# Kernel tuning notes

Measured on AMD Instinct MI355X. Metric: run time of the kernel, lower is better.

The kernel has to match this reference:

```python
import jax, jax.numpy as jnp
import numpy as np

BLOCK = 32  # block_h == block_w (triton blocksparse requires square blocks)


def setup_inputs() -> dict:
    key = jax.random.key(0)
    kq, kk, kv, kb, km = jax.random.split(key, 5)
    B, H, S, D = 2, 16, 2048, 64
    query = jax.random.normal(kq, (B, H, S, D), dtype=jnp.float32)
    key_t = jax.random.normal(kk, (B, H, S, D), dtype=jnp.float32)
    value = jax.random.normal(kv, (B, H, S, D), dtype=jnp.float32)
    # grouped Conv2d bias (default bias=True, left at random init in the module)
    conv_bias = jax.random.normal(kb, (H,), dtype=jnp.float32)
    mask = jax.random.randint(km, (H, S, S), 0, 2, dtype=jnp.int32)
    return {"query": query, "key": key_t, "value": value,
            "conv_bias": conv_bias, "mask": mask}


def reference(query, key, value, conv_bias, mask):
    # --- build data-dependent block mask (grouped conv, weight==1, stride==kernel==BLOCK) ---
    H, S, _ = mask.shape
    nb = S // BLOCK
    block_sum = mask.reshape(H, nb, BLOCK, nb, BLOCK).sum(axis=(2, 4)).astype(jnp.float32)
    block_mask = (block_sum + conv_bias[:, None, None]) > 0  # [H, nb, nb]

    # element-level allowed pattern: block active AND causal (triton sparse_softmax is_causal=True)
    elem = jnp.repeat(jnp.repeat(block_mask, BLOCK, axis=1), BLOCK, axis=2)  # [H, S, S]
    causal = jnp.tril(jnp.ones((S, S), dtype=bool))
    allow = elem & causal  # [H, S, S]

    # --- sparse SDD: QK^T restricted to active blocks (scale = 1.0) ---
    scores = jnp.einsum('bhsd,bhtd->bhst', query, key)  # [B, H, S, S]

    # --- sparse causal softmax: disallowed positions are -inf; fully-masked rows -> 0 ---
    NEG = jnp.float32(-1e30)
    s = jnp.where(allow[None], scores, NEG)
    m = jnp.max(s, axis=-1, keepdims=True)
    p = jnp.where(allow[None], jnp.exp(s - m), 0.0)
    denom = jnp.sum(p, axis=-1, keepdims=True)
    w = jnp.where(denom > 0, p / denom, 0.0)

    # --- sparse DSD: attention @ V (absent blocks contribute zero) ---
    return jnp.einsum('bhst,bhtd->bhsd', w, value)
```

## Files before the change

### kernel.cpp

```cpp
#include <hip/hip_runtime.h>
#include <hip/hip_bf16.h>


typedef _Float16 f16_t;
typedef f16_t  f16x8  __attribute__((ext_vector_type(8)));
typedef __fp16 fp16x2 __attribute__((ext_vector_type(2)));
typedef float  f32x4  __attribute__((ext_vector_type(4)));
typedef float  f32x16 __attribute__((ext_vector_type(16)));
typedef int    i32x4  __attribute__((ext_vector_type(4)));
typedef int    i32x2  __attribute__((ext_vector_type(2)));
typedef unsigned int u32x4 __attribute__((ext_vector_type(4)));

constexpr int Bc = 2, Hc = 16, Sc = 2048, Dc = 64;
constexpr int NB = Sc / 32;
constexpr float LOG2E = 1.4426950408889634f;
constexpr size_t FRAG_BH = (size_t)NB * 4 * 64 * 8;

__device__ inline f32x16 mfma32(f16x8 a, f16x8 b, f32x16 c) {
    return __builtin_amdgcn_mfma_f32_32x32x16_f16(a, b, c, 0, 0, 0);
}
__device__ inline float fexp2(float x) { return __builtin_amdgcn_exp2f(x); }

union UB { u32x4 u; f16x8 v; };
union PK { fp16x2 h; unsigned int u; };

#if __has_builtin(__builtin_amdgcn_permlane32_swap)
#define HAVE_PLSWAP 1
__device__ inline i32x2 plswap(unsigned int a, unsigned int b) {
    return __builtin_amdgcn_permlane32_swap((int)a, (int)b, false, false);
}
__device__ inline float xhalf_max(float x) {
    i32x2 s = plswap((unsigned int)__float_as_int(x), (unsigned int)__float_as_int(x));
    return fmaxf(__int_as_float(s[0]), __int_as_float(s[1]));
}
__device__ inline float xhalf_sum(float x) {
    i32x2 s = plswap((unsigned int)__float_as_int(x), (unsigned int)__float_as_int(x));
    return __int_as_float(s[0]) + __int_as_float(s[1]);
}
#else
#define HAVE_PLSWAP 0
__device__ inline float xhalf_max(float x) { return fmaxf(x, __shfl_xor(x, 32)); }
__device__ inline float xhalf_sum(float x) { return x + __shfl_xor(x, 32); }
#endif

__global__ __launch_bounds__(256) void k_prep(const float* __restrict__ K,
                                              const float* __restrict__ V,
                                              const int* __restrict__ mask,
                                              const float* __restrict__ bias,
                                              f16_t* __restrict__ khf,
                                              f16_t* __restrict__ vaf,
                                              unsigned char* __restrict__ bm) {
    __shared__ f16_t tile[32 * 66];
    const int bid = blockIdx.x;
    const int t   = threadIdx.x;
    if (bid < 2048) {
        const int bh = bid >> 6, kb = bid & 63;
        const float* src = K + ((size_t)bh * Sc + (size_t)kb * 32) * Dc;
        {
            int r = t >> 3, c8 = (t & 7) * 8;
            f32x4 a = *(const f32x4*)(src + r * Dc + c8);
            f32x4 b = *(const f32x4*)(src + r * Dc + c8 + 4);
            float xs[8] = {a[0], a[1], a[2], a[3], b[0], b[1], b[2], b[3]};
#pragma unroll
            for (int j = 0; j < 8; j++) tile[r * 66 + c8 + j] = (f16_t)xs[j];
        }
        __syncthreads();
        {
            int kc = t >> 6, lane = t & 63, l31 = lane & 31, hi2 = (lane >> 5) & 1;
            f16x8 frag;
#pragma unroll
            for (int j = 0; j < 8; j++)
                frag[j] = tile[l31 * 66 + kc * 16 + hi2 * 8 + j];
            *(f16x8*)(khf + (((size_t)(bh * NB + kb) * 4 + kc) * 64 + lane) * 8) = frag;
        }
    } else if (bid < 4096) {
        const int b2 = bid - 2048;
        const int bh = b2 >> 6, kb = b2 & 63;
        const float* src = V + ((size_t)bh * Sc + (size_t)kb * 32) * Dc;
        {
            int r = t >> 3, c8 = (t & 7) * 8;
            f32x4 a = *(const f32x4*)(src + r * Dc + c8);
            f32x4 b = *(const f32x4*)(src + r * Dc + c8 + 4);
            float xs[8] = {a[0], a[1], a[2], a[3], b[0], b[1], b[2], b[3]};
#pragma unroll
            for (int j = 0; j < 8; j++) tile[r * 66 + c8 + j] = (f16_t)xs[j];
        }
        __syncthreads();
        {
            int f = t >> 6, lane = t & 63, l31 = lane & 31, hi2 = (lane >> 5) & 1;
            int tt = f >> 1, c = f & 1;
            f16x8 frag;
#pragma unroll
            for (int j = 0; j < 8; j++)
                frag[j] = tile[(c * 16 + hi2 * 8 + j) * 66 + tt * 32 + l31];
            *(f16x8*)(vaf + (((size_t)(bh * NB + kb) * 4 + f) * 64 + lane) * 8) = frag;
        }
    } else {
        const int b3 = bid - 4096;
        const int h  = b3 >> 6;
        const int br = b3 & 63;
        float bv = bias[h];
        unsigned char* outp = bm + ((size_t)h * NB + br) * NB;
        if (bv > 0.f) {
            if (t < NB) outp[t] = 1;
            return;
        }
        int bc0 = t >> 3;
        int bc1 = 32 + bc0;
        const int* base = mask + ((size_t)h * Sc + (size_t)br * 32) * (size_t)Sc;
        const int* p0 = base + 4 * t;
        const int* p1 = base + 1024 + 4 * t;
        bool d0 = (bc0 <= br), d1 = (bc1 <= br);
        int acc0 = 0, acc1 = 0;
        if (d0) {
#pragma unroll
            for (int r = 0; r < 4; r++) {
                i32x4 vv = *(const i32x4*)(p0 + (size_t)r * Sc);
                acc0 += vv[0] + vv[1] + vv[2] + vv[3];
            }
        }
        if (d1) {
#pragma unroll
            for (int r = 0; r < 4; r++) {
                i32x4 vv = *(const i32x4*)(p1 + (size_t)r * Sc);
                acc1 += vv[0] + vv[1] + vv[2] + vv[3];
            }
        }
        int g0 = acc0, g1 = acc1;
#pragma unroll
        for (int off = 1; off < 8; off <<= 1) {
            g0 += __shfl_xor(g0, off);
            g1 += __shfl_xor(g1, off);
        }
        bool act0 = (float)g0 + bv > 0.f;
        bool act1 = (float)g1 + bv > 0.f;
        if (d0 && !act0) {
            for (int r = 4; r < 32; r++) {
                i32x4 vv = *(const i32x4*)(p0 + (size_t)r * Sc);
                acc0 += vv[0] + vv[1] + vv[2] + vv[3];
            }
            int s = acc0;
#pragma unroll
            for (int off = 1; off < 8; off <<= 1) s += __shfl_xor(s, off);
            act0 = (float)s + bv > 0.f;
        }
        if (d1 && !act1) {
            for (int r = 4; r < 32; r++) {
                i32x4 vv = *(const i32x4*)(p1 + (size_t)r * Sc);
                acc1 += vv[0] + vv[1] + vv[2] + vv[3];
            }
            int s = acc1;
#pragma unroll
            for (int off = 1; off < 8; off <<= 1) s += __shfl_xor(s, off);
            act1 = (float)s + bv > 0.f;
        }
        if ((t & 7) == 0) {
            if (d0) outp[bc0] = act0 ? 1 : 0;
            if (d1) outp[bc1] = act1 ? 1 : 0;
        }
    }
}

#if HAVE_PLSWAP
#define EXCHANGE_P(PB, B0, B1) do {                                            \
        i32x2 e0_ = plswap(PB[0], PB[2]);                                      \
        i32x2 e1_ = plswap(PB[1], PB[3]);                                      \
        i32x2 e2_ = plswap(PB[4], PB[6]);                                      \
        i32x2 e3_ = plswap(PB[5], PB[7]);                                      \
        B0.u[0] = (unsigned int)e0_[0]; B0.u[1] = (unsigned int)e1_[0];        \
        B0.u[2] = (unsigned int)e0_[1]; B0.u[3] = (unsigned int)e1_[1];        \
        B1.u[0] = (unsigned int)e2_[0]; B1.u[1] = (unsigned int)e3_[0];        \
        B1.u[2] = (unsigned int)e2_[1]; B1.u[3] = (unsigned int)e3_[1];        \
} while (0)
#else
#define EXCHANGE_P(PB, B0, B1) do {                                            \
        unsigned int qb_[8];                                                   \
        _Pragma("unroll")                                                      \
        for (int i_ = 0; i_ < 8; i_++)                                         \
            qb_[i_] = (unsigned int)__shfl_xor((int)PB[i_], 32);               \
        B0.u[0] = hi ? qb_[2] : PB[0]; B0.u[1] = hi ? qb_[3] : PB[1];          \
        B0.u[2] = hi ? PB[2] : qb_[0]; B0.u[3] = hi ? PB[3] : qb_[1];          \
        B1.u[0] = hi ? qb_[6] : PB[4]; B1.u[1] = hi ? qb_[7] : PB[5];          \
        B1.u[2] = hi ? PB[6] : qb_[4]; B1.u[3] = hi ? PB[7] : qb_[5];          \
} while (0)
#endif

#define CORE(OT0, OT1, MR, LR, QH, BROW, kb_) do {                             \
        f32x16 st;                                                             \
        _Pragma("unroll")                                                      \
        for (int r_ = 0; r_ < 16; r_++) st[r_] = 0.f;                          \
        _Pragma("unroll")                                                      \
        for (int kc_ = 0; kc_ < 4; kc_++)                                      \
            st = mfma32(kbuf_[kc_], QH[kc_], st);                              \
        if ((kb_) == (BROW)) {                                                 \
            _Pragma("unroll")                                                  \
            for (int r_ = 0; r_ < 16; r_++) {                                  \
                int kvl_ = (r_ & 3) + 8 * (r_ >> 2) + 4 * hi;                  \
                if (kvl_ > l31) st[r_] = -1e30f;                               \
            }                                                                  \
        }                                                                      \
        float a0_ = fmaxf(fmaxf(st[0], st[1]), st[2]);                         \
        float a1_ = fmaxf(fmaxf(st[3], st[4]), st[5]);                         \
        float a2_ = fmaxf(fmaxf(st[6], st[7]), st[8]);                         \
        float a3_ = fmaxf(fmaxf(st[9], st[10]), st[11]);                       \
        float a4_ = fmaxf(fmaxf(st[12], st[13]), st[14]);                      \
        float b0m_ = fmaxf(fmaxf(a0_, a1_), a2_);                              \
        float b1m_ = fmaxf(fmaxf(a3_, a4_), st[15]);                           \
        float mx_ = xhalf_max(fmaxf(b0m_, b1m_));                              \
        if (__ballot(mx_ > MR + 11.0f)) {                                      \
            float mn_ = fmaxf(MR, mx_);                                        \
            float al_ = fexp2(MR - mn_);                                       \
            MR = mn_;                                                          \
            LR *= al_;                                                         \
            OT0 *= al_; OT1 *= al_;                                            \
        }                                                                      \
        _Pragma("unroll")                                                      \
        for (int r_ = 0; r_ < 16; r_++) st[r_] = fexp2(st[r_] - MR);           \
        {                                                                      \
            float s0 = (st[0] + st[1]) + (st[2] + st[3]);                      \
            float s1 = (st[4] + st[5]) + (st[6] + st[7]);                      \
            float s2 = (st[8] + st[9]) + (st[10] + st[11]);                    \
            float s3 = (st[12] + st[13]) + (st[14] + st[15]);                  \
            LR += ((s0 + s1) + (s2 + s3));                                     \
        }                                                                      \
        unsigned int pb_[8];                                                   \
        _Pragma("unroll")                                                      \
        for (int i_ = 0; i_ < 8; i_++) {                                       \
            PK pk_;                                                            \
            pk_.h = __builtin_amdgcn_cvt_pkrtz(st[2 * i_], st[2 * i_ + 1]);    \
            pb_[i_] = pk_.u;                                                   \
        }                                                                      \
        UB b0_, b1_;                                                           \
        EXCHANGE_P(pb_, b0_, b1_);                                             \
        OT0 = mfma32(va_[0][0], b0_.v, OT0);                                   \
        OT0 = mfma32(va_[0][1], b1_.v, OT0);                                   \
        OT1 = mfma32(va_[1][0], b0_.v, OT1);                                   \
        OT1 = mfma32(va_[1][1], b1_.v, OT1);                                   \
} while (0)

#define QLOAD(QH, q0_) do {                                                    \
        const float* qr_ = q_ptr + (size_t)((q0_) + l31) * Dc + hi * 8;        \
        _Pragma("unroll")                                                      \
        for (int kc_ = 0; kc_ < 4; kc_++) {                                    \
            f32x4 a_ = *(const f32x4*)(qr_ + kc_ * 16);                        \
            f32x4 b_ = *(const f32x4*)(qr_ + kc_ * 16 + 4);                    \
            float xs_[8] = {a_[0], a_[1], a_[2], a_[3], b_[0], b_[1], b_[2], b_[3]}; \
            _Pragma("unroll")                                                  \
            for (int j_ = 0; j_ < 8; j_++) QH[kc_][j_] = (f16_t)(xs_[j_] * LOG2E); \
        }                                                                      \
} while (0)

__global__ __launch_bounds__(128, 4) void k_attn(const float* __restrict__ Q,
                                                 const f16_t* __restrict__ KHF,
                                                 const f16_t* __restrict__ VAF,
                                                 const unsigned char* __restrict__ BM,
                                                 float* __restrict__ Out) {
    __shared__ float lds_o[64 * 33];
    __shared__ float lds_m[32];
    __shared__ float lds_l[32];

    const int qi   = 63 - (int)(blockIdx.x >> 5);
    const int bh   = blockIdx.x & 31;
    const int h    = bh & (Hc - 1);
    const int w    = threadIdx.x >> 6;
    const int lane = threadIdx.x & 63;
    const int l31  = lane & 31, hi = lane >> 5;

    const size_t bh_off = (size_t)bh * Sc * Dc;
    const float* q_ptr  = Q + bh_off;
    const f16_t* khfp   = KHF + (size_t)bh * FRAG_BH;
    const f16_t* vafp   = VAF + (size_t)bh * FRAG_BH;

    const int q0   = qi * 32;
    const int brow = qi;
    const unsigned char* bmrow = BM + ((size_t)h * NB + brow) * NB;
    const unsigned long long actmask = __ballot(bmrow[lane] != 0);

    f16x8 qh[4];
    QLOAD(qh, q0);

    f32x16 ot0, ot1;
#pragma unroll
    for (int r = 0; r < 16; r++) { ot0[r] = 0.f; ot1[r] = 0.f; }
    float mrow = -INFINITY, lrow = 0.f;

    for (int kb = w; kb <= brow; kb += 2) {
        if (!((actmask >> kb) & 1ull)) continue;
        f16x8 kbuf_[4];
#pragma unroll
        for (int kc = 0; kc < 4; kc++)
            kbuf_[kc] = *(const f16x8*)(khfp + (((size_t)kb * 4 + kc) * 64 + lane) * 8);
        f16x8 va_[2][2];
#pragma unroll
        for (int t = 0; t < 2; t++)
#pragma unroll
            for (int c = 0; c < 2; c++)
                va_[t][c] = *(const f16x8*)(vafp + (((size_t)kb * 4 + t * 2 + c) * 64 + lane) * 8);
        CORE(ot0, ot1, mrow, lrow, qh, brow, kb);
    }

    float lsum = xhalf_sum(lrow);
    if (w == 1) {
#pragma unroll
        for (int r = 0; r < 16; r++) {
            int d0 = (r & 3) + 8 * (r >> 2) + 4 * hi;
            lds_o[d0 * 33 + l31]        = ot0[r];
            lds_o[(d0 + 32) * 33 + l31] = ot1[r];
        }
        if (hi == 0) { lds_m[l31] = mrow; lds_l[l31] = lsum; }
    }
    __syncthreads();
    if (w == 0) {
        float m1 = lds_m[l31], l1 = lds_l[l31];
        float mm = fmaxf(mrow, m1);
        float a0 = (mrow > -1e37f) ? fexp2(mrow - mm) : 0.f;
        float a1 = (m1   > -1e37f) ? fexp2(m1   - mm) : 0.f;
        float lt = lsum * a0 + l1 * a1;
        float inv = (lt > 0.f) ? (1.f / lt) : 0.f;
        float* op = Out + bh_off + (size_t)(q0 + l31) * Dc;
#pragma unroll
        for (int g = 0; g < 4; g++) {
            f32x4 w0, w1;
#pragma unroll
            for (int jj = 0; jj < 4; jj++) {
                int r = g * 4 + jj;
                int d0 = jj + 8 * g + 4 * hi;
                w0[jj] = (ot0[r] * a0 + lds_o[d0 * 33 + l31] * a1) * inv;
                w1[jj] = (ot1[r] * a0 + lds_o[(d0 + 32) * 33 + l31] * a1) * inv;
            }
            *(f32x4*)(op + g * 8 + hi * 4)      = w0;
            *(f32x4*)(op + 32 + g * 8 + hi * 4) = w1;
        }
    }
}

extern "C" void kernel_launch(void* const* d_in, const int* in_sizes, int n_in,
                              void* d_out, int out_size, void* d_ws, size_t ws_size,
                              hipStream_t stream) {
    const float* Q    = (const float*)d_in[0];
    const float* K    = (const float*)d_in[1];
    const float* V    = (const float*)d_in[2];
    const float* bias = (const float*)d_in[3];
    const int*   mask = (const int*)d_in[4];
    float* out = (float*)d_out;

    char* ws = (char*)d_ws;
    f16_t* khf = (f16_t*)ws;
    f16_t* vaf = (f16_t*)(ws + (size_t)32 * FRAG_BH * 2);
    unsigned char* bm = (unsigned char*)(ws + (size_t)64 * FRAG_BH * 2);

    k_prep <<<5120, 256, 0, stream>>>(K, V, mask, bias, khf, vaf, bm);
    k_attn <<<Bc * Hc * NB, 128, 0, stream>>>(Q, khf, vaf, bm, out);
}
```

Baseline: 49.16 us.

## Share K/V blocks across four query rows per workgroup via LDS double buffering

Each 256-thread workgroup now handles four query block-rows (p, 31-p, 32+p, 63-p), one per wave, chosen so the causal work is balanced. The K/V fragment blocks are staged cooperatively through a double-buffered LDS buffer with register prefetch, so each block is loaded from global memory once and used by all four waves. The old split of keys across two waves, with its LDS merge of partial softmax state, is removed. In exchange there is a __syncthreads per key block, waves sit idle on blocks outside their causal range or inactive, and grid size drops by 4x.

```diff
diff --git a/kernel.cpp b/kernel.cpp
--- a/kernel.cpp
+++ b/kernel.cpp
@@ -185,7 +185,17 @@
 } while (0)
 #endif
 
-#define CORE(OT0, OT1, MR, LR, QH, BROW, kb_) do {                             \
+#define CORE(OT0, OT1, MR, LR, QH, BROW, kb_, SK, SV) do {                     \
+        f16x8 kbuf_[4];                                                        \
+        _Pragma("unroll")                                                      \
+        for (int kc_ = 0; kc_ < 4; kc_++)                                      \
+            kbuf_[kc_] = *(const f16x8*)((SK) + kc_ * 512 + lane * 8);         \
+        f16x8 va_[2][2];                                                       \
+        _Pragma("unroll")                                                      \
+        for (int t_ = 0; t_ < 2; t_++)                                         \
+            _Pragma("unroll")                                                  \
+            for (int c_ = 0; c_ < 2; c_++)                                     \
+                va_[t_][c_] = *(const f16x8*)((SV) + (t_ * 2 + c_) * 512 + lane * 8); \
         f32x16 st;                                                             \
         _Pragma("unroll")                                                      \
         for (int r_ = 0; r_ < 16; r_++) st[r_] = 0.f;                          \
@@ -250,20 +260,19 @@
         }                                                                      \
 } while (0)
 
-__global__ __launch_bounds__(128, 4) void k_attn(const float* __restrict__ Q,
+__global__ __launch_bounds__(256, 2) void k_attn(const float* __restrict__ Q,
                                                  const f16_t* __restrict__ KHF,
                                                  const f16_t* __restrict__ VAF,
                                                  const unsigned char* __restrict__ BM,
                                                  float* __restrict__ Out) {
-    __shared__ float lds_o[64 * 33];
-    __shared__ float lds_m[32];
-    __shared__ float lds_l[32];
-
-    const int qi   = 63 - (int)(blockIdx.x >> 5);
-    const int bh   = blockIdx.x & 31;
-    const int h    = bh & (Hc - 1);
-    const int w    = threadIdx.x >> 6;
-    const int lane = threadIdx.x & 63;
+    __shared__ f16_t sbuf[2][4096];
+
+    const int p  = blockIdx.x >> 5;
+    const int bh = blockIdx.x & 31;
+    const int h  = bh & (Hc - 1);
+    const int t  = threadIdx.x;
+    const int w  = t >> 6;
+    const int lane = t & 63;
     const int l31  = lane & 31, hi = lane >> 5;
 
     const size_t bh_off = (size_t)bh * Sc * Dc;
@@ -271,8 +280,10 @@
     const f16_t* khfp   = KHF + (size_t)bh * FRAG_BH;
     const f16_t* vafp   = VAF + (size_t)bh * FRAG_BH;
 
+    const int qi = (w == 0) ? p : (w == 1) ? 31 - p : (w == 2) ? 32 + p : 63 - p;
+    const int brow = qi;
+    const int kend = 63 - p;
     const int q0   = qi * 32;
-    const int brow = qi;
     const unsigned char* bmrow = BM + ((size_t)h * NB + brow) * NB;
     const unsigned long long actmask = __ballot(bmrow[lane] != 0);
 
@@ -284,53 +295,37 @@
     for (int r = 0; r < 16; r++) { ot0[r] = 0.f; ot1[r] = 0.f; }
     float mrow = -INFINITY, lrow = 0.f;
 
-    for (int kb = w; kb <= brow; kb += 2) {
-        if (!((actmask >> kb) & 1ull)) continue;
-        f16x8 kbuf_[4];
-#pragma unroll
-        for (int kc = 0; kc < 4; kc++)
-            kbuf_[kc] = *(const f16x8*)(khfp + (((size_t)kb * 4 + kc) * 64 + lane) * 8);
-        f16x8 va_[2][2];
-#pragma unroll
-        for (int t = 0; t < 2; t++)
-#pragma unroll
-            for (int c = 0; c < 2; c++)
-                va_[t][c] = *(const f16x8*)(vafp + (((size_t)kb * 4 + t * 2 + c) * 64 + lane) * 8);
-        CORE(ot0, ot1, mrow, lrow, qh, brow, kb);
+    f16x8 rK = *(const f16x8*)(khfp + (size_t)0 * 2048 + t * 8);
+    f16x8 rV = *(const f16x8*)(vafp + (size_t)0 * 2048 + t * 8);
+    for (int kb = 0; kb <= kend; kb++) {
+        f16_t* sk = &sbuf[kb & 1][0];
+        f16_t* sv = &sbuf[kb & 1][2048];
+        *(f16x8*)(sk + t * 8) = rK;
+        *(f16x8*)(sv - 2048 + 2048 + t * 8) = rV;
+        if (kb < kend) {
+            rK = *(const f16x8*)(khfp + (size_t)(kb + 1) * 2048 + t * 8);
+            rV = *(const f16x8*)(vafp + (size_t)(kb + 1) * 2048 + t * 8);
+        }
+        __syncthreads();
+        if (kb <= brow && ((actmask >> kb) & 1ull)) {
+            CORE(ot0, ot1, mrow, lrow, qh, brow, kb, sk, sv);
+        }
     }
 
     float lsum = xhalf_sum(lrow);
-    if (w == 1) {
-#pragma unroll
-        for (int r = 0; r < 16; r++) {
-            int d0 = (r & 3) + 8 * (r >> 2) + 4 * hi;
-            lds_o[d0 * 33 + l31]        = ot0[r];
-            lds_o[(d0 + 32) * 33 + l31] = ot1[r];
-        }
-        if (hi == 0) { lds_m[l31] = mrow; lds_l[l31] = lsum; }
-    }
-    __syncthreads();
-    if (w == 0) {
-        float m1 = lds_m[l31], l1 = lds_l[l31];
-        float mm = fmaxf(mrow, m1);
-        float a0 = (mrow > -1e37f) ? fexp2(mrow - mm) : 0.f;
-        float a1 = (m1   > -1e37f) ? fexp2(m1   - mm) : 0.f;
-        float lt = lsum * a0 + l1 * a1;
-        float inv = (lt > 0.f) ? (1.f / lt) : 0.f;
-        float* op = Out + bh_off + (size_t)(q0 + l31) * Dc;
-#pragma unroll
-        for (int g = 0; g < 4; g++) {
-            f32x4 w0, w1;
-#pragma unroll
-            for (int jj = 0; jj < 4; jj++) {
-                int r = g * 4 + jj;
-                int d0 = jj + 8 * g + 4 * hi;
-                w0[jj] = (ot0[r] * a0 + lds_o[d0 * 33 + l31] * a1) * inv;
-                w1[jj] = (ot1[r] * a0 + lds_o[(d0 + 32) * 33 + l31] * a1) * inv;
-            }
-            *(f32x4*)(op + g * 8 + hi * 4)      = w0;
-            *(f32x4*)(op + 32 + g * 8 + hi * 4) = w1;
-        }
+    float inv  = (lsum > 0.f) ? (1.f / lsum) : 0.f;
+    float* op  = Out + bh_off + (size_t)(q0 + l31) * Dc;
+#pragma unroll
+    for (int g = 0; g < 4; g++) {
+        f32x4 w0, w1;
+#pragma unroll
+        for (int jj = 0; jj < 4; jj++) {
+            int r = g * 4 + jj;
+            w0[jj] = ot0[r] * inv;
+            w1[jj] = ot1[r] * inv;
+        }
+        *(f32x4*)(op + g * 8 + hi * 4)      = w0;
+        *(f32x4*)(op + 32 + g * 8 + hi * 4) = w1;
     }
 }
 
@@ -350,5 +345,5 @@
     unsigned char* bm = (unsigned char*)(ws + (size_t)64 * FRAG_BH * 2);
 
     k_prep <<<5120, 256, 0, stream>>>(K, V, mask, bias, khf, vaf, bm);
-    k_attn <<<Bc * Hc * NB, 128, 0, stream>>>(Q, khf, vaf, bm, out);
-}
+    k_attn <<<Hc * Bc * (NB / 4), 256, 0, stream>>>(Q, khf, vaf, bm, out);
+}
```

Result: slower. 55.31 us (+12.5%).
